# Kernel tuning notes

Measured on AMD Instinct MI355X. Metric: run time of the kernel, lower is better.

Reference implementation:

```python
import jax, jax.numpy as jnp
import numpy as np


def _lstm_dir(x, w_ih, w_hh, b, reverse):
    # x: [S,B,I], w_ih: [4H,I], w_hh: [4H,H], b: [4H]. torch gate order i,f,g,o.
    H = w_hh.shape[1]
    gx = jnp.einsum('sbi,gi->sbg', x, w_ih) + b  # precompute input projections
    B = x.shape[1]
    h0 = jnp.zeros((B, H), x.dtype)

    def step(carry, g):
        h, c = carry
        z = g + h @ w_hh.T
        i, f, gg, o = jnp.split(z, 4, axis=-1)
        c = jax.nn.sigmoid(f) * c + jax.nn.sigmoid(i) * jnp.tanh(gg)
        h = jax.nn.sigmoid(o) * jnp.tanh(c)
        return (h, c), h

    (hT, _), hs = jax.lax.scan(step, (h0, h0), gx, reverse=reverse)
    return hs, hT  # hs: [S,B,H] in original time order; hT final hidden


def _bilstm_layer(x, w_ih, w_hh, b):
    # x: [S,B,I]; params stacked [2, ...] for (forward, backward)
    hs_f, hT_f = _lstm_dir(x, w_ih[0], w_hh[0], b[0], reverse=False)
    hs_b, hT_b = _lstm_dir(x, w_ih[1], w_hh[1], b[1], reverse=True)
    return jnp.concatenate([hs_f, hs_b], axis=-1), hT_f, hT_b


def reference(tokens, emb, w_ih0, w_hh0, b0, w_ih1, w_hh1, b1, fc1_w, fc1_b, fc2_w, fc2_b):
    # tokens: [B,S] int; embedding lookup (frozen table)
    x = emb[tokens]                       # [B,S,E]
    x = jnp.transpose(x, (1, 0, 2))       # [S,B,E] time-major for scan
    h0_seq, _, _ = _bilstm_layer(x, w_ih0, w_hh0, b0)          # [S,B,2H]
    _, hT_f, hT_b = _bilstm_layer(h0_seq, w_ih1, w_hh1, b1)    # final layer
    out = jnp.concatenate([hT_f, hT_b], axis=-1)               # [B,2H]
    out = jax.nn.relu(out @ fc1_w.T + fc1_b)
    return out @ fc2_w.T + fc2_b          # [B,2]


def setup_inputs() -> dict:
    key = jax.random.key(0)
    ks = jax.random.split(key, 13)
    B, S, V, E, H = 256, 512, 50000, 300, 128
    s = 0.05
    return {
        'tokens': jax.random.randint(ks[0], (B, S), 0, V, dtype=jnp.int32),
        'emb':    jax.random.normal(ks[1], (V, E), jnp.float32) * s,
        'w_ih0':  jax.random.normal(ks[2], (2, 4 * H, E), jnp.float32) * s,
        'w_hh0':  jax.random.normal(ks[3], (2, 4 * H, H), jnp.float32) * s,
        'b0':     jax.random.normal(ks[4], (2, 4 * H), jnp.float32) * s,
        'w_ih1':  jax.random.normal(ks[5], (2, 4 * H, 2 * H), jnp.float32) * s,
        'w_hh1':  jax.random.normal(ks[6], (2, 4 * H, H), jnp.float32) * s,
        'b1':     jax.random.normal(ks[7], (2, 4 * H), jnp.float32) * s,
        'fc1_w':  jax.random.normal(ks[8], (H, 2 * H), jnp.float32) * s,
        'fc1_b':  jax.random.normal(ks[9], (H,), jnp.float32) * s,
        'fc2_w':  jax.random.normal(ks[10], (2, H), jnp.float32) * s,
        'fc2_b':  jax.random.normal(ks[11], (2,), jnp.float32) * s,
    }
```

## Files before the change

kernel.cpp:

```cpp
#include <hip/hip_runtime.h>

#define S_LEN 512
#define BATCH 256
#define EMB_D 300
#define EMB_PAD 320
#define HID 128
#define SB (S_LEN*BATCH)
#define CH 128
#define NCH 4

typedef __attribute__((ext_vector_type(8))) short bf16x8;
typedef __attribute__((ext_vector_type(4))) float f32x4;
typedef unsigned short u16;
typedef unsigned int   u32;

__device__ __forceinline__ float b2f(u16 u) {
    union { u32 i; float f; } v; v.i = ((u32)u) << 16; return v.f;
}
__device__ __forceinline__ u16 f2b(float f) {
    union { float f; u32 i; } v; v.f = f;
    u32 r = v.i + 0x7fffu + ((v.i >> 16) & 1u);
    return (u16)(r >> 16);
}
__device__ __forceinline__ float sigf(float x) {
    return __builtin_amdgcn_rcpf(1.f + __expf(-x));
}
__device__ __forceinline__ float tanhf_fast(float x) {
    float e = __expf(2.f * x);
    return 1.f - 2.f * __builtin_amdgcn_rcpf(e + 1.f);
}

__global__ void k_detect(const u16* __restrict__ emb_u, int* __restrict__ flag) {
    __shared__ int cnt;
    if (threadIdx.x == 0) cnt = 0;
    __syncthreads();
    float v = b2f(emb_u[2 * threadIdx.x + 64]);
    float a = fabsf(v);
    if (a > 1e-4f && a < 16.f) atomicAdd(&cnt, 1);
    __syncthreads();
    if (threadIdx.x == 0) *flag = (cnt > 128) ? 1 : 0;
}

__global__ void k_packw(const void* __restrict__ src, u16* __restrict__ dst,
                        int Kin, int Kpad, int total, const int* __restrict__ flag) {
    int i = blockIdx.x * 256 + threadIdx.x;
    if (i >= total) return;
    int n = i / Kpad, k = i - n * Kpad;
    int d = n >> 9, r = n & 511, j = r >> 2, t = r & 3;
    size_t si = (size_t)((d << 9) + (t << 7) + j) * Kin + k;
    u16 v = 0;
    if (k < Kin) {
        if (*flag) v = ((const u16*)src)[si];
        else       v = f2b(((const float*)src)[si]);
    }
    dst[i] = v;
}

__global__ void k_packb(const void* __restrict__ src, float* __restrict__ dst,
                        const int* __restrict__ flag) {
    int i = blockIdx.x * 256 + threadIdx.x;
    if (i >= 1024) return;
    int d = i >> 9, r = i & 511, j = r >> 2, t = r & 3;
    size_t si = (d << 9) + (t << 7) + j;
    dst[i] = (*flag) ? b2f(((const u16*)src)[si]) : ((const float*)src)[si];
}

template<int KPAD, bool EMBED>
__global__ __launch_bounds__(256) void k_gemm(const int* __restrict__ tok,
                                              const void* __restrict__ Asrc,
                                              const u16* __restrict__ W,
                                              const float* __restrict__ bias,
                                              u16* __restrict__ C,
                                              const int* __restrict__ flag,
                                              int soff0, int soff1) {
    __shared__ __align__(16) u16 As[64 * 40];
    __shared__ __align__(16) u16 Bs[64 * 40];
    const int tid  = threadIdx.x;
    const int by   = blockIdx.y;
    const int dir  = by >> 3;
    const int n0   = (by & 7) * 64;
    const int m0   = blockIdx.x * 64;
    const int soff = dir ? soff1 : soff0;
    const size_t mg0 = (size_t)soff * BATCH;
    const int w    = tid >> 6, lane = tid & 63, quad = lane >> 4, l16 = lane & 15;
    const int mq   = (w >> 1) * 32, nq = (w & 1) * 32;
    const int row  = tid >> 2, seg = tid & 3;

    bool is_bf = true;
    size_t arow_off = 0;
    if constexpr (EMBED) {
        size_t m = mg0 + m0 + row;
        int s = (int)(m >> 8), b = (int)(m & 255);
        is_bf = (*flag != 0);
        arow_off = (size_t)tok[b * S_LEN + s] * EMB_D;
    } else {
        arow_off = (mg0 + m0 + row) * KPAD;
    }
    const u16* brow = W + (size_t)(dir * 512 + n0 + row) * KPAD;

    f32x4 acc[2][2] = {};
    const int KSTEPS = KPAD / 32;
#pragma unroll
    for (int kk = 0; kk < KSTEPS; ++kk) {
        uint4 va, vb;
        if constexpr (EMBED) {
            u32 u[4];
            if (is_bf) {
                const u16* ar = (const u16*)Asrc + arow_off;
#pragma unroll
                for (int i = 0; i < 4; ++i) {
                    int c = kk * 32 + seg * 8 + 2 * i;
                    u[i] = (c < EMB_D) ? *(const u32*)(ar + c) : 0u;
                }
            } else {
                const float* ar = (const float*)Asrc + arow_off;
#pragma unroll
                for (int i = 0; i < 4; ++i) {
                    int c = kk * 32 + seg * 8 + 2 * i;
                    if (c < EMB_D) {
                        float2 f = *(const float2*)(ar + c);
                        u[i] = (u32)f2b(f.x) | ((u32)f2b(f.y) << 16);
                    } else u[i] = 0u;
                }
            }
            va.x = u[0]; va.y = u[1]; va.z = u[2]; va.w = u[3];
        } else {
            va = *((const uint4*)((const u16*)Asrc + arow_off) + kk * 4 + seg);
        }
        vb = *((const uint4*)brow + kk * 4 + seg);
        __syncthreads();
        *(uint4*)(As + row * 40 + seg * 8) = va;
        *(uint4*)(Bs + row * 40 + seg * 8) = vb;
        __syncthreads();
        bf16x8 af[2], bfr[2];
#pragma unroll
        for (int mt = 0; mt < 2; ++mt)
            af[mt] = *(const bf16x8*)(As + (mq + mt * 16 + l16) * 40 + quad * 8);
#pragma unroll
        for (int nt = 0; nt < 2; ++nt)
            bfr[nt] = *(const bf16x8*)(Bs + (nq + nt * 16 + l16) * 40 + quad * 8);
#pragma unroll
        for (int mt = 0; mt < 2; ++mt)
#pragma unroll
            for (int nt = 0; nt < 2; ++nt)
                acc[mt][nt] = __builtin_amdgcn_mfma_f32_16x16x32_bf16(af[mt], bfr[nt], acc[mt][nt], 0, 0, 0);
    }
#pragma unroll
    for (int mt = 0; mt < 2; ++mt)
#pragma unroll
        for (int nt = 0; nt < 2; ++nt)
#pragma unroll
            for (int r = 0; r < 4; ++r) {
                int mloc = m0 + mq + mt * 16 + quad * 4 + r;
                int nloc = n0 + nq + nt * 16 + l16;
                float v = acc[mt][nt][r] + bias[dir * 512 + nloc];
                C[(size_t)dir * CH * BATCH * 512 + (size_t)mloc * 512 + nloc] = f2b(v);
            }
}

template<bool IS_L0>
__global__ __launch_bounds__(1024) void k_lstm(const u16* __restrict__ gxc,
                                               const u16* __restrict__ Whp,
                                               u16* __restrict__ h0seq, float* __restrict__ hT,
                                               u16* __restrict__ hstate, float* __restrict__ cstate,
                                               int k) {
    const int tid  = threadIdx.x;
    const int d    = blockIdx.x >> 4;
    const int bg   = blockIdx.x & 15;
    const int wv   = tid >> 6, lane = tid & 63, quad = lane >> 4, col = lane & 15;
    const int soff = (d == 0) ? CH * k : CH * (NCH - 1 - k);

    __shared__ __align__(16) u16 hbuf[2][16][136];
    __shared__ __align__(16) u16 gxb [2][16][520];

    for (int i = tid; i < 2 * 16 * 136; i += 1024) ((u16*)hbuf)[i] = 0;
    __syncthreads();
    if (k > 0) {
        for (int i = tid; i < 16 * 128; i += 1024) {
            int bl = i >> 7, j = i & 127;
            hbuf[0][bl][j] = hstate[((size_t)d * BATCH + bg * 16 + bl) * 128 + j];
        }
    }

    const u16* Wd = Whp + (size_t)d * 512 * 128;
    bf16x8 wf[2][4];
#pragma unroll
    for (int mt = 0; mt < 2; ++mt)
#pragma unroll
        for (int ks = 0; ks < 4; ++ks)
            wf[mt][ks] = *(const bf16x8*)(Wd + (size_t)(((wv * 2 + mt) * 16) + col) * 128 + ks * 32 + quad * 8);

    const u16* gxd = gxc + (size_t)d * CH * BATCH * 512;
    auto sloc = [&](int si) { return (d == 0) ? si : (CH - 1 - si); };

    auto prefetch = [&](int si, int P) {
        const u16* g0 = gxd + ((size_t)sloc(si) * BATCH + bg * 16 + wv) * 512 + lane * 8;
        __builtin_amdgcn_global_load_lds((const __attribute__((address_space(1))) void*)g0,
            (__attribute__((address_space(3))) void*)&gxb[P][wv][0], 16, 0, 0);
    };

    float c[2];
#pragma unroll
    for (int mt = 0; mt < 2; ++mt)
        c[mt] = (k > 0) ? cstate[((size_t)d * BATCH + bg * 16 + col) * 128 + (wv * 2 + mt) * 4 + quad] : 0.f;

    auto step = [&](int si, int P) {
        if (si + 1 < CH) prefetch(si + 1, P ^ 1);
        if constexpr (IS_L0) {
            if (si > 0) {
                int sp = soff + ((d == 0) ? (si - 1) : (CH - si));
                ushort2 hv = *(const ushort2*)&hbuf[P][wv][lane * 2];
                *(ushort2*)(h0seq + ((size_t)sp * BATCH + bg * 16 + wv) * 256 + (d << 7) + lane * 2) = hv;
            }
        }
        bf16x8 hf[4];
#pragma unroll
        for (int ks = 0; ks < 4; ++ks)
            hf[ks] = *(const bf16x8*)&hbuf[P][col][ks * 32 + quad * 8];
        f32x4 z[2];
#pragma unroll
        for (int mt = 0; mt < 2; ++mt) {
            ushort4 gv = *(const ushort4*)&gxb[P][col][(wv * 2 + mt) * 16 + quad * 4];
            z[mt][0] = b2f(gv.x); z[mt][1] = b2f(gv.y); z[mt][2] = b2f(gv.z); z[mt][3] = b2f(gv.w);
        }
#pragma unroll
        for (int ks = 0; ks < 4; ++ks)
#pragma unroll
            for (int mt = 0; mt < 2; ++mt)
                z[mt] = __builtin_amdgcn_mfma_f32_16x16x32_bf16(wf[mt][ks], hf[ks], z[mt], 0, 0, 0);
#pragma unroll
        for (int mt = 0; mt < 2; ++mt) {
            float iv = sigf(z[mt][0]), fv = sigf(z[mt][1]);
            float gg = tanhf_fast(z[mt][2]), ov = sigf(z[mt][3]);
            c[mt] = fv * c[mt] + iv * gg;
            float hv = ov * tanhf_fast(c[mt]);
            const int j = (wv * 2 + mt) * 4 + quad;
            hbuf[P ^ 1][col][j] = f2b(hv);
            if constexpr (!IS_L0) {
                if (k == NCH - 1 && si == CH - 1)
                    hT[((size_t)d * BATCH + bg * 16 + col) * 128 + j] = hv;
            }
        }
        __syncthreads();
    };

    prefetch(0, 0);
    __syncthreads();

    for (int si = 0; si < CH; si += 2) {
        step(si, 0);
        step(si + 1, 1);
    }

    if constexpr (IS_L0) {
        int sp = soff + ((d == 0) ? (CH - 1) : 0);
        ushort2 hv = *(const ushort2*)&hbuf[0][wv][lane * 2];
        *(ushort2*)(h0seq + ((size_t)sp * BATCH + bg * 16 + wv) * 256 + (d << 7) + lane * 2) = hv;
    }
    if (k < NCH - 1) {
        for (int i = tid; i < 16 * 128; i += 1024) {
            int bl = i >> 7, j = i & 127;
            hstate[((size_t)d * BATCH + bg * 16 + bl) * 128 + j] = hbuf[0][bl][j];
        }
#pragma unroll
        for (int mt = 0; mt < 2; ++mt)
            cstate[((size_t)d * BATCH + bg * 16 + col) * 128 + (wv * 2 + mt) * 4 + quad] = c[mt];
    }
}

__global__ void k_fc(const float* __restrict__ hT,
                     const void* __restrict__ fc1w, const void* __restrict__ fc1b,
                     const void* __restrict__ fc2w, const void* __restrict__ fc2b,
                     void* __restrict__ out, const int* __restrict__ flag) {
    int b = blockIdx.x, j = threadIdx.x;
    bool is_bf = (*flag != 0);
    __shared__ float u[128];
    float a = is_bf ? b2f(((const u16*)fc1b)[j]) : ((const float*)fc1b)[j];
    for (int k = 0; k < 256; ++k) {
        float x = hT[((size_t)(k >> 7) * BATCH + b) * 128 + (k & 127)];
        float w = is_bf ? b2f(((const u16*)fc1w)[j * 256 + k]) : ((const float*)fc1w)[j * 256 + k];
        a += x * w;
    }
    u[j] = fmaxf(a, 0.f);
    __syncthreads();
    if (j < 2) {
        float a2 = is_bf ? b2f(((const u16*)fc2b)[j]) : ((const float*)fc2b)[j];
        for (int q = 0; q < 128; ++q) {
            float w = is_bf ? b2f(((const u16*)fc2w)[j * 128 + q]) : ((const float*)fc2w)[j * 128 + q];
            a2 += u[q] * w;
        }
        if (is_bf) ((u16*)out)[b * 2 + j] = f2b(a2);
        else       ((float*)out)[b * 2 + j] = a2;
    }
}

extern "C" void kernel_launch(void* const* d_in, const int* in_sizes, int n_in,
                              void* d_out, int out_size, void* d_ws, size_t ws_size,
                              hipStream_t stream) {
    const int*  tok   = (const int*)d_in[0];
    const void* emb   = d_in[1];
    const void* w_ih0 = d_in[2];
    const void* w_hh0 = d_in[3];
    const void* b0    = d_in[4];
    const void* w_ih1 = d_in[5];
    const void* w_hh1 = d_in[6];
    const void* b1    = d_in[7];
    const void* fc1w  = d_in[8];
    const void* fc1b  = d_in[9];
    const void* fc2w  = d_in[10];
    const void* fc2b  = d_in[11];

    char* ws = (char*)d_ws;
    size_t off = 0;
    auto alloc = [&](size_t bytes) -> void* {
        void* p = ws + off; off += (bytes + 255) & ~(size_t)255; return p;
    };
    int*   flag   = (int*)alloc(256);
    u16*   Wp0    = (u16*)alloc(1024 * 320 * 2);
    u16*   Wp1    = (u16*)alloc(1024 * 256 * 2);
    u16*   Whp0   = (u16*)alloc(1024 * 128 * 2);
    u16*   Whp1   = (u16*)alloc(1024 * 128 * 2);
    float* bp0    = (float*)alloc(1024 * 4);
    float* bp1    = (float*)alloc(1024 * 4);
    float* hT     = (float*)alloc((size_t)2 * BATCH * 128 * 4);
    u16*   hstate = (u16*)alloc((size_t)2 * BATCH * 128 * 2);
    float* cstate = (float*)alloc((size_t)2 * BATCH * 128 * 4);
    u16*   h0seq  = (u16*)alloc((size_t)SB * 256 * 2);
    u16*   gxc    = (u16*)alloc((size_t)2 * CH * BATCH * 512 * 2);

    k_detect<<<1, 256, 0, stream>>>((const u16*)emb, flag);

    k_packw<<<(1024 * 320 + 255) / 256, 256, 0, stream>>>(w_ih0, Wp0, 300, 320, 1024 * 320, flag);
    k_packw<<<(1024 * 256 + 255) / 256, 256, 0, stream>>>(w_ih1, Wp1, 256, 256, 1024 * 256, flag);
    k_packw<<<(1024 * 128 + 255) / 256, 256, 0, stream>>>(w_hh0, Whp0, 128, 128, 1024 * 128, flag);
    k_packw<<<(1024 * 128 + 255) / 256, 256, 0, stream>>>(w_hh1, Whp1, 128, 128, 1024 * 128, flag);
    k_packb<<<4, 256, 0, stream>>>(b0, bp0, flag);
    k_packb<<<4, 256, 0, stream>>>(b1, bp1, flag);

    const dim3 gg(CH * BATCH / 64, 16);
    for (int k = 0; k < NCH; ++k) {
        int so0 = CH * k, so1 = CH * (NCH - 1 - k);
        k_gemm<320, true ><<<gg, 256, 0, stream>>>(tok, emb, Wp0, bp0, gxc, flag, so0, so1);
        k_lstm<true ><<<32, 1024, 0, stream>>>(gxc, Whp0, h0seq, nullptr, hstate, cstate, k);
    }
    for (int k = 0; k < NCH; ++k) {
        int so0 = CH * k, so1 = CH * (NCH - 1 - k);
        k_gemm<256, false><<<gg, 256, 0, stream>>>(nullptr, h0seq, Wp1, bp1, gxc, flag, so0, so1);
        k_lstm<false><<<32, 1024, 0, stream>>>(gxc, Whp1, nullptr, hT, hstate, cstate, k);
    }
    k_fc<<<256, 128, 0, stream>>>(hT, fc1w, fc1b, fc2w, fc2b, d_out, flag);
}
```

Baseline: 1.803 ms.

## Fuse chunked input GEMM with LSTM recurrence to overlap next-chunk projection

```diff
diff --git a/kernel.cpp b/kernel.cpp
--- a/kernel.cpp
+++ b/kernel.cpp
@@ -8,6 +8,8 @@
 #define SB (S_LEN*BATCH)
 #define CH 128
 #define NCH 4
+#define GXC_DIR ((size_t)CH*BATCH*512)
+#define SMEM_BYTES 86016
 
 typedef __attribute__((ext_vector_type(8))) short bf16x8;
 typedef __attribute__((ext_vector_type(4))) float f32x4;
@@ -65,80 +67,196 @@
     dst[i] = (*flag) ? b2f(((const u16*)src)[si]) : ((const float*)src)[si];
 }
 
-template<int KPAD, bool EMBED>
-__global__ __launch_bounds__(256) void k_gemm(const int* __restrict__ tok,
-                                              const void* __restrict__ Asrc,
-                                              const u16* __restrict__ W,
-                                              const float* __restrict__ bias,
-                                              u16* __restrict__ C,
-                                              const int* __restrict__ flag,
-                                              int soff0, int soff1) {
-    __shared__ __align__(16) u16 As[64 * 40];
-    __shared__ __align__(16) u16 Bs[64 * 40];
-    const int tid  = threadIdx.x;
-    const int by   = blockIdx.y;
-    const int dir  = by >> 3;
-    const int n0   = (by & 7) * 64;
-    const int m0   = blockIdx.x * 64;
-    const int soff = dir ? soff1 : soff0;
+template<int KPAD, bool EMBED, bool IS_L0>
+__global__ __launch_bounds__(1024) void k_fused(
+    const int* __restrict__ tok, const void* __restrict__ Asrc,
+    const u16* __restrict__ W, const float* __restrict__ bias,
+    u16* __restrict__ gx_out, const u16* __restrict__ gx_in,
+    const u16* __restrict__ Whp,
+    u16* __restrict__ h0seq, float* __restrict__ hT,
+    u16* __restrict__ hstate, float* __restrict__ cstate,
+    int k, int nlstm, int soff0g, int soff1g, const int* __restrict__ flag)
+{
+    __shared__ __align__(16) char smem[SMEM_BYTES];
+    const int tid = threadIdx.x;
+
+    if ((int)blockIdx.x < nlstm) {
+        u16* hb = (u16*)smem;
+        u16* gb = (u16*)(smem + 8704);
+        const int d    = blockIdx.x >> 4;
+        const int bg   = blockIdx.x & 15;
+        const int wv   = tid >> 6, lane = tid & 63, quad = lane >> 4, col = lane & 15;
+        const int soff = (d == 0) ? CH * k : CH * (NCH - 1 - k);
+
+        for (int i = tid; i < 2 * 16 * 136; i += 1024) hb[i] = 0;
+        __syncthreads();
+        if (k > 0) {
+            for (int i = tid; i < 16 * 128; i += 1024) {
+                int bl = i >> 7, j = i & 127;
+                hb[bl * 136 + j] = hstate[((size_t)d * BATCH + bg * 16 + bl) * 128 + j];
+            }
+        }
+
+        const u16* Wd = Whp + (size_t)d * 512 * 128;
+        bf16x8 wf[2][4];
+#pragma unroll
+        for (int mt = 0; mt < 2; ++mt)
+#pragma unroll
+            for (int ks = 0; ks < 4; ++ks)
+                wf[mt][ks] = *(const bf16x8*)(Wd + (size_t)(((wv * 2 + mt) * 16) + col) * 128 + ks * 32 + quad * 8);
+
+        const u16* gxd = gx_in + (size_t)d * GXC_DIR;
+        auto sloc = [&](int si) { return (d == 0) ? si : (CH - 1 - si); };
+        auto prefetch = [&](int si, int P) {
+            const u16* g0 = gxd + ((size_t)sloc(si) * BATCH + bg * 16 + wv) * 512 + lane * 8;
+            __builtin_amdgcn_global_load_lds((const __attribute__((address_space(1))) void*)g0,
+                (__attribute__((address_space(3))) void*)(gb + (P * 16 + wv) * 520), 16, 0, 0);
+        };
+
+        float c[2];
+#pragma unroll
+        for (int mt = 0; mt < 2; ++mt)
+            c[mt] = (k > 0) ? cstate[((size_t)d * BATCH + bg * 16 + col) * 128 + (wv * 2 + mt) * 4 + quad] : 0.f;
+
+        auto step = [&](int si, int P) {
+            if (si + 1 < CH) prefetch(si + 1, P ^ 1);
+            if constexpr (IS_L0) {
+                if (si > 0) {
+                    int sp = soff + ((d == 0) ? (si - 1) : (CH - si));
+                    ushort2 hv = *(const ushort2*)(hb + (P * 16 + wv) * 136 + lane * 2);
+                    *(ushort2*)(h0seq + ((size_t)sp * BATCH + bg * 16 + wv) * 256 + (d << 7) + lane * 2) = hv;
+                }
+            }
+            bf16x8 hf[4];
+#pragma unroll
+            for (int ks = 0; ks < 4; ++ks)
+                hf[ks] = *(const bf16x8*)(hb + (P * 16 + col) * 136 + ks * 32 + quad * 8);
+            f32x4 z[2];
+#pragma unroll
+            for (int mt = 0; mt < 2; ++mt) {
+                ushort4 gv = *(const ushort4*)(gb + (P * 16 + col) * 520 + (wv * 2 + mt) * 16 + quad * 4);
+                z[mt][0] = b2f(gv.x); z[mt][1] = b2f(gv.y); z[mt][2] = b2f(gv.z); z[mt][3] = b2f(gv.w);
+            }
+#pragma unroll
+            for (int ks = 0; ks < 4; ++ks)
+#pragma unroll
+                for (int mt = 0; mt < 2; ++mt)
+                    z[mt] = __builtin_amdgcn_mfma_f32_16x16x32_bf16(wf[mt][ks], hf[ks], z[mt], 0, 0, 0);
+#pragma unroll
+            for (int mt = 0; mt < 2; ++mt) {
+                float iv = sigf(z[mt][0]), fv = sigf(z[mt][1]);
+                float gg = tanhf_fast(z[mt][2]), ov = sigf(z[mt][3]);
+                c[mt] = fv * c[mt] + iv * gg;
+                float hv = ov * tanhf_fast(c[mt]);
+                const int j = (wv * 2 + mt) * 4 + quad;
+                hb[((P ^ 1) * 16 + col) * 136 + j] = f2b(hv);
+                if constexpr (!IS_L0) {
+                    if (k == NCH - 1 && si == CH - 1)
+                        hT[((size_t)d * BATCH + bg * 16 + col) * 128 + j] = hv;
+                }
+            }
+            __syncthreads();
+        };
+
+        prefetch(0, 0);
+        __syncthreads();
+
+        for (int si = 0; si < CH; si += 2) {
+            step(si, 0);
+            step(si + 1, 1);
+        }
+
+        if constexpr (IS_L0) {
+            int sp = soff + ((d == 0) ? (CH - 1) : 0);
+            ushort2 hv = *(const ushort2*)(hb + wv * 136 + lane * 2);
+            *(ushort2*)(h0seq + ((size_t)sp * BATCH + bg * 16 + wv) * 256 + (d << 7) + lane * 2) = hv;
+        }
+        if (k < NCH - 1) {
+            for (int i = tid; i < 16 * 128; i += 1024) {
+                int bl = i >> 7, j = i & 127;
+                hstate[((size_t)d * BATCH + bg * 16 + bl) * 128 + j] = hb[bl * 136 + j];
+            }
+#pragma unroll
+            for (int mt = 0; mt < 2; ++mt)
+                cstate[((size_t)d * BATCH + bg * 16 + col) * 128 + (wv * 2 + mt) * 4 + quad] = c[mt];
+        }
+        return;
+    }
+
+    const int g   = (int)blockIdx.x - nlstm;
+    u16* As = (u16*)smem;
+    u16* Bs = (u16*)(smem + 10240);
+    const int gy  = g >> 8;
+    const int m0  = (g & 255) * 128;
+    const int dir = gy >> 2;
+    const int n0  = (gy & 3) * 128;
+    const int soff = dir ? soff1g : soff0g;
     const size_t mg0 = (size_t)soff * BATCH;
-    const int w    = tid >> 6, lane = tid & 63, quad = lane >> 4, l16 = lane & 15;
-    const int mq   = (w >> 1) * 32, nq = (w & 1) * 32;
-    const int row  = tid >> 2, seg = tid & 3;
+    const int w = tid >> 6, lane = tid & 63, quad = lane >> 4, l16 = lane & 15;
+    const int wm = w >> 2, wn = w & 3;
+    const int crow = (tid & 511) >> 2, cseg = tid & 3;
+    const bool isA = tid < 512;
 
     bool is_bf = true;
     size_t arow_off = 0;
-    if constexpr (EMBED) {
-        size_t m = mg0 + m0 + row;
-        int s = (int)(m >> 8), b = (int)(m & 255);
-        is_bf = (*flag != 0);
-        arow_off = (size_t)tok[b * S_LEN + s] * EMB_D;
+    const u16* brow = nullptr;
+    if (isA) {
+        if constexpr (EMBED) {
+            size_t m = mg0 + m0 + crow;
+            int s = (int)(m >> 8), b = (int)(m & 255);
+            is_bf = (*flag != 0);
+            arow_off = (size_t)tok[b * S_LEN + s] * EMB_D;
+        } else {
+            arow_off = (mg0 + m0 + crow) * KPAD;
+        }
     } else {
-        arow_off = (mg0 + m0 + row) * KPAD;
-    }
-    const u16* brow = W + (size_t)(dir * 512 + n0 + row) * KPAD;
+        brow = W + (size_t)(dir * 512 + n0 + crow) * KPAD;
+    }
 
     f32x4 acc[2][2] = {};
     const int KSTEPS = KPAD / 32;
 #pragma unroll
     for (int kk = 0; kk < KSTEPS; ++kk) {
-        uint4 va, vb;
-        if constexpr (EMBED) {
-            u32 u[4];
-            if (is_bf) {
-                const u16* ar = (const u16*)Asrc + arow_off;
-#pragma unroll
-                for (int i = 0; i < 4; ++i) {
-                    int c = kk * 32 + seg * 8 + 2 * i;
-                    u[i] = (c < EMB_D) ? *(const u32*)(ar + c) : 0u;
+        uint4 v;
+        if (isA) {
+            if constexpr (EMBED) {
+                u32 u[4];
+                if (is_bf) {
+                    const u16* ar = (const u16*)Asrc + arow_off;
+#pragma unroll
+                    for (int i = 0; i < 4; ++i) {
+                        int cc = kk * 32 + cseg * 8 + 2 * i;
+                        u[i] = (cc < EMB_D) ? *(const u32*)(ar + cc) : 0u;
+                    }
+                } else {
+                    const float* ar = (const float*)Asrc + arow_off;
+#pragma unroll
+                    for (int i = 0; i < 4; ++i) {
+                        int cc = kk * 32 + cseg * 8 + 2 * i;
+                        if (cc < EMB_D) {
+                            float2 f = *(const float2*)(ar + cc);
+                            u[i] = (u32)f2b(f.x) | ((u32)f2b(f.y) << 16);
+                        } else u[i] = 0u;
+                    }
                 }
+                v.x = u[0]; v.y = u[1]; v.z = u[2]; v.w = u[3];
             } else {
-                const float* ar = (const float*)Asrc + arow_off;
-#pragma unroll
-                for (int i = 0; i < 4; ++i) {
-                    int c = kk * 32 + seg * 8 + 2 * i;
-                    if (c < EMB_D) {
-                        float2 f = *(const float2*)(ar + c);
-                        u[i] = (u32)f2b(f.x) | ((u32)f2b(f.y) << 16);
-                    } else u[i] = 0u;
-                }
-            }
-            va.x = u[0]; va.y = u[1]; va.z = u[2]; va.w = u[3];
+                v = *((const uint4*)((const u16*)Asrc + arow_off) + kk * 4 + cseg);
+            }
         } else {
-            va = *((const uint4*)((const u16*)Asrc + arow_off) + kk * 4 + seg);
-        }
-        vb = *((const uint4*)brow + kk * 4 + seg);
+            v = *((const uint4*)brow + kk * 4 + cseg);
+        }
         __syncthreads();
-        *(uint4*)(As + row * 40 + seg * 8) = va;
-        *(uint4*)(Bs + row * 40 + seg * 8) = vb;
+        if (isA) *(uint4*)(As + crow * 40 + cseg * 8) = v;
+        else     *(uint4*)(Bs + crow * 40 + cseg * 8) = v;
         __syncthreads();
         bf16x8 af[2], bfr[2];
 #pragma unroll
         for (int mt = 0; mt < 2; ++mt)
-            af[mt] = *(const bf16x8*)(As + (mq + mt * 16 + l16) * 40 + quad * 8);
+            af[mt] = *(const bf16x8*)(As + (wm * 32 + mt * 16 + l16) * 40 + quad * 8);
 #pragma unroll
         for (int nt = 0; nt < 2; ++nt)
-            bfr[nt] = *(const bf16x8*)(Bs + (nq + nt * 16 + l16) * 40 + quad * 8);
+            bfr[nt] = *(const bf16x8*)(Bs + (wn * 32 + nt * 16 + l16) * 40 + quad * 8);
 #pragma unroll
         for (int mt = 0; mt < 2; ++mt)
 #pragma unroll
@@ -151,121 +269,11 @@
         for (int nt = 0; nt < 2; ++nt)
 #pragma unroll
             for (int r = 0; r < 4; ++r) {
-                int mloc = m0 + mq + mt * 16 + quad * 4 + r;
-                int nloc = n0 + nq + nt * 16 + l16;
-                float v = acc[mt][nt][r] + bias[dir * 512 + nloc];
-                C[(size_t)dir * CH * BATCH * 512 + (size_t)mloc * 512 + nloc] = f2b(v);
-            }
-}
-
-template<bool IS_L0>
-__global__ __launch_bounds__(1024) void k_lstm(const u16* __restrict__ gxc,
-                                               const u16* __restrict__ Whp,
-                                               u16* __restrict__ h0seq, float* __restrict__ hT,
-                                               u16* __restrict__ hstate, float* __restrict__ cstate,
-                                               int k) {
-    const int tid  = threadIdx.x;
-    const int d    = blockIdx.x >> 4;
-    const int bg   = blockIdx.x & 15;
-    const int wv   = tid >> 6, lane = tid & 63, quad = lane >> 4, col = lane & 15;
-    const int soff = (d == 0) ? CH * k : CH * (NCH - 1 - k);
-
-    __shared__ __align__(16) u16 hbuf[2][16][136];
-    __shared__ __align__(16) u16 gxb [2][16][520];
-
-    for (int i = tid; i < 2 * 16 * 136; i += 1024) ((u16*)hbuf)[i] = 0;
-    __syncthreads();
-    if (k > 0) {
-        for (int i = tid; i < 16 * 128; i += 1024) {
-            int bl = i >> 7, j = i & 127;
-            hbuf[0][bl][j] = hstate[((size_t)d * BATCH + bg * 16 + bl) * 128 + j];
-        }
-    }
-
-    const u16* Wd = Whp + (size_t)d * 512 * 128;
-    bf16x8 wf[2][4];
-#pragma unroll
-    for (int mt = 0; mt < 2; ++mt)
-#pragma unroll
-        for (int ks = 0; ks < 4; ++ks)
-            wf[mt][ks] = *(const bf16x8*)(Wd + (size_t)(((wv * 2 + mt) * 16) + col) * 128 + ks * 32 + quad * 8);
-
-    const u16* gxd = gxc + (size_t)d * CH * BATCH * 512;
-    auto sloc = [&](int si) { return (d == 0) ? si : (CH - 1 - si); };
-
-    auto prefetch = [&](int si, int P) {
-        const u16* g0 = gxd + ((size_t)sloc(si) * BATCH + bg * 16 + wv) * 512 + lane * 8;
-        __builtin_amdgcn_global_load_lds((const __attribute__((address_space(1))) void*)g0,
-            (__attribute__((address_space(3))) void*)&gxb[P][wv][0], 16, 0, 0);
-    };
-
-    float c[2];
-#pragma unroll
-    for (int mt = 0; mt < 2; ++mt)
-        c[mt] = (k > 0) ? cstate[((size_t)d * BATCH + bg * 16 + col) * 128 + (wv * 2 + mt) * 4 + quad] : 0.f;
-
-    auto step = [&](int si, int P) {
-        if (si + 1 < CH) prefetch(si + 1, P ^ 1);
-        if constexpr (IS_L0) {
-            if (si > 0) {
-                int sp = soff + ((d == 0) ? (si - 1) : (CH - si));
-                ushort2 hv = *(const ushort2*)&hbuf[P][wv][lane * 2];
-                *(ushort2*)(h0seq + ((size_t)sp * BATCH + bg * 16 + wv) * 256 + (d << 7) + lane * 2) = hv;
-            }
-        }
-        bf16x8 hf[4];
-#pragma unroll
-        for (int ks = 0; ks < 4; ++ks)
-            hf[ks] = *(const bf16x8*)&hbuf[P][col][ks * 32 + quad * 8];
-        f32x4 z[2];
-#pragma unroll
-        for (int mt = 0; mt < 2; ++mt) {
-            ushort4 gv = *(const ushort4*)&gxb[P][col][(wv * 2 + mt) * 16 + quad * 4];
-            z[mt][0] = b2f(gv.x); z[mt][1] = b2f(gv.y); z[mt][2] = b2f(gv.z); z[mt][3] = b2f(gv.w);
-        }
-#pragma unroll
-        for (int ks = 0; ks < 4; ++ks)
-#pragma unroll
-            for (int mt = 0; mt < 2; ++mt)
-                z[mt] = __builtin_amdgcn_mfma_f32_16x16x32_bf16(wf[mt][ks], hf[ks], z[mt], 0, 0, 0);
-#pragma unroll
-        for (int mt = 0; mt < 2; ++mt) {
-            float iv = sigf(z[mt][0]), fv = sigf(z[mt][1]);
-            float gg = tanhf_fast(z[mt][2]), ov = sigf(z[mt][3]);
-            c[mt] = fv * c[mt] + iv * gg;
-            float hv = ov * tanhf_fast(c[mt]);
-            const int j = (wv * 2 + mt) * 4 + quad;
-            hbuf[P ^ 1][col][j] = f2b(hv);
-            if constexpr (!IS_L0) {
-                if (k == NCH - 1 && si == CH - 1)
-                    hT[((size_t)d * BATCH + bg * 16 + col) * 128 + j] = hv;
-            }
-        }
-        __syncthreads();
-    };
-
-    prefetch(0, 0);
-    __syncthreads();
-
-    for (int si = 0; si < CH; si += 2) {
-        step(si, 0);
-        step(si + 1, 1);
-    }
-
-    if constexpr (IS_L0) {
-        int sp = soff + ((d == 0) ? (CH - 1) : 0);
-        ushort2 hv = *(const ushort2*)&hbuf[0][wv][lane * 2];
-        *(ushort2*)(h0seq + ((size_t)sp * BATCH + bg * 16 + wv) * 256 + (d << 7) + lane * 2) = hv;
-    }
-    if (k < NCH - 1) {
-        for (int i = tid; i < 16 * 128; i += 1024) {
-            int bl = i >> 7, j = i & 127;
-            hstate[((size_t)d * BATCH + bg * 16 + bl) * 128 + j] = hbuf[0][bl][j];
-        }
-#pragma unroll
-        for (int mt = 0; mt < 2; ++mt)
-            cstate[((size_t)d * BATCH + bg * 16 + col) * 128 + (wv * 2 + mt) * 4 + quad] = c[mt];
-    }
+                int mloc = m0 + wm * 32 + mt * 16 + quad * 4 + r;
+                int nloc = n0 + wn * 32 + nt * 16 + l16;
+                float vv = acc[mt][nt][r] + bias[dir * 512 + nloc];
+                gx_out[(size_t)dir * GXC_DIR + (size_t)mloc * 512 + nloc] = f2b(vv);
+            }
 }
 
 __global__ void k_fc(const float* __restrict__ hT,
@@ -326,7 +334,10 @@
     u16*   hstate = (u16*)alloc((size_t)2 * BATCH * 128 * 2);
     float* cstate = (float*)alloc((size_t)2 * BATCH * 128 * 4);
     u16*   h0seq  = (u16*)alloc((size_t)SB * 256 * 2);
-    u16*   gxc    = (u16*)alloc((size_t)2 * CH * BATCH * 512 * 2);
+    size_t bufb   = 2 * GXC_DIR * sizeof(u16);
+    u16*   gxcA   = (u16*)alloc(bufb);
+    bool overlap  = ws_size >= off + bufb;
+    u16*   gxcB   = overlap ? (u16*)alloc(bufb) : gxcA;
 
     k_detect<<<1, 256, 0, stream>>>((const u16*)emb, flag);
 
@@ -337,16 +348,48 @@
     k_packb<<<4, 256, 0, stream>>>(b0, bp0, flag);
     k_packb<<<4, 256, 0, stream>>>(b1, bp1, flag);
 
-    const dim3 gg(CH * BATCH / 64, 16);
-    for (int k = 0; k < NCH; ++k) {
-        int so0 = CH * k, so1 = CH * (NCH - 1 - k);
-        k_gemm<320, true ><<<gg, 256, 0, stream>>>(tok, emb, Wp0, bp0, gxc, flag, so0, so1);
-        k_lstm<true ><<<32, 1024, 0, stream>>>(gxc, Whp0, h0seq, nullptr, hstate, cstate, k);
-    }
-    for (int k = 0; k < NCH; ++k) {
-        int so0 = CH * k, so1 = CH * (NCH - 1 - k);
-        k_gemm<256, false><<<gg, 256, 0, stream>>>(nullptr, h0seq, Wp1, bp1, gxc, flag, so0, so1);
-        k_lstm<false><<<32, 1024, 0, stream>>>(gxc, Whp1, nullptr, hT, hstate, cstate, k);
+    const int NG = 2048;
+
+    if (overlap) {
+        k_fused<320, true, true><<<NG, 1024, 0, stream>>>(
+            tok, emb, Wp0, bp0, gxcA, gxcA, Whp0, h0seq, nullptr, hstate, cstate,
+            0, 0, 0, CH * (NCH - 1), flag);
+        for (int k = 0; k < NCH; ++k) {
+            int ng = (k < NCH - 1) ? NG : 0;
+            u16* gin  = (k & 1) ? gxcB : gxcA;
+            u16* gout = (k & 1) ? gxcA : gxcB;
+            k_fused<320, true, true><<<32 + ng, 1024, 0, stream>>>(
+                tok, emb, Wp0, bp0, gout, gin, Whp0, h0seq, nullptr, hstate, cstate,
+                k, 32, CH * (k + 1), CH * (NCH - 2 - k), flag);
+        }
+        k_fused<256, false, false><<<NG, 1024, 0, stream>>>(
+            nullptr, h0seq, Wp1, bp1, gxcA, gxcA, Whp1, nullptr, hT, hstate, cstate,
+            0, 0, 0, CH * (NCH - 1), flag);
+        for (int k = 0; k < NCH; ++k) {
+            int ng = (k < NCH - 1) ? NG : 0;
+            u16* gin  = (k & 1) ? gxcB : gxcA;
+            u16* gout = (k & 1) ? gxcA : gxcB;
+            k_fused<256, false, false><<<32 + ng, 1024, 0, stream>>>(
+                nullptr, h0seq, Wp1, bp1, gout, gin, Whp1, nullptr, hT, hstate, cstate,
+                k, 32, CH * (k + 1), CH * (NCH - 2 - k), flag);
+        }
+    } else {
+        for (int k = 0; k < NCH; ++k) {
+            k_fused<320, true, true><<<NG, 1024, 0, stream>>>(
+                tok, emb, Wp0, bp0, gxcA, gxcA, Whp0, h0seq, nullptr, hstate, cstate,
+                0, 0, CH * k, CH * (NCH - 1 - k), flag);
+            k_fused<320, true, true><<<32, 1024, 0, stream>>>(
+                tok, emb, Wp0, bp0, gxcA, gxcA, Whp0, h0seq, nullptr, hstate, cstate,
+                k, 32, 0, 0, flag);
+        }
+        for (int k = 0; k < NCH; ++k) {
+            k_fused<256, false, false><<<NG, 1024, 0, stream>>>(
+                nullptr, h0seq, Wp1, bp1, gxcA, gxcA, Whp1, nullptr, hT, hstate, cstate,
+                0, 0, CH * k, CH * (NCH - 1 - k), flag);
+            k_fused<256, false, false><<<32, 1024, 0, stream>>>(
+                nullptr, h0seq, Wp1, bp1, gxcA, gxcA, Whp1, nullptr, hT, hstate, cstate,
+                k, 32, 0, 0, flag);
+        }
     }
     k_fc<<<256, 128, 0, stream>>>(hT, fc1w, fc1b, fc2w, fc2b, d_out, flag);
 }
```

After: 1.560 ms. 13.4% less time.
